# Optimization experiments

Measured on AMD Instinct MI355X. Metric: run time of the kernel, lower is better.

## Reference

```python
import jax, jax.numpy as jnp
import numpy as np

B = 256
MAXN = 1000
EPG = 7813
K, K1, K2 = 30, 3, 27


def setup_inputs():
    counts = np.where(np.arange(B) % 2 == 0, MAXN, 800).astype(np.int64)
    NT = int(counts.sum())  # 230400 nodes
    offsets = np.concatenate([[0], np.cumsum(counts)[:-1]]).astype(np.int64)
    batch = np.repeat(np.arange(B, dtype=np.int64), counts)
    rng = np.random.RandomState(0)
    E = B * EPG
    gid = np.repeat(np.arange(B), EPG)
    n = counts[gid]
    src = (rng.rand(E) * n).astype(np.int64)
    dst = (src + 1 + (rng.rand(E) * (n - 1)).astype(np.int64)) % n  # no self loops
    edge_index = np.stack([offsets[gid] + src, offsets[gid] + dst])
    key = jax.random.key(0)
    ks = jax.random.split(key, 8)
    def lin(k, fi, fo):
        return jax.random.normal(k, (fi, fo), jnp.float32) / np.sqrt(float(fi))
    return {
        'x': jax.random.normal(ks[0], (NT, 128), jnp.float32),
        'edge_index': jnp.asarray(edge_index),
        'batch': jnp.asarray(batch),
        'W1': lin(ks[1], 128, 64), 'b1': jnp.zeros(64, jnp.float32),
        'W2': lin(ks[2], 64, 64), 'b2': jnp.zeros(64, jnp.float32),
        'W3': lin(ks[3], 64, 64), 'b3': jnp.zeros(64, jnp.float32),
        'W4': lin(ks[4], 64, 1), 'b4': jnp.zeros(1, jnp.float32),
        'conv5_w': jax.random.normal(ks[5], (64, 1, 193), jnp.float32) / np.sqrt(193.0),
        'conv5_b': jnp.zeros(64, jnp.float32),
        'conv6_w': jax.random.normal(ks[6], (64, 64, 5), jnp.float32) / np.sqrt(320.0),
        'conv6_b': jnp.zeros(64, jnp.float32),
        'fc_w': lin(ks[7], 704, 1600), 'fc_b': jnp.zeros(1600, jnp.float32),
        'num_graphs': B,
        'max_num_nodes': MAXN,
    }


def _gcn(h_in, W, b, row, col, w_edge, self_w, N):
    h = h_in @ W
    agg = jax.ops.segment_sum(h[row] * w_edge[:, None], col, num_segments=N)
    return agg + self_w[:, None] * h + b


def _forward(x, edge_index, batch, W1, b1, W2, b2, W3, b3, W4, b4, conv5_w, conv5_b, conv6_w, conv6_b, fc_w, fc_b, num_graphs, max_num_nodes):
    N = x.shape[0]
    row, col = edge_index[0], edge_index[1]
    # GCN symmetric normalization with implicit self loops: deg = in-degree + 1
    deg = jax.ops.segment_sum(jnp.ones(row.shape[0], x.dtype), col, num_segments=N) + 1.0
    dis = jax.lax.rsqrt(deg)
    w_edge = dis[row] * dis[col]
    self_w = dis * dis
    x1 = jnp.tanh(_gcn(x, W1, b1, row, col, w_edge, self_w, N))
    x2 = jnp.tanh(_gcn(x1, W2, b2, row, col, w_edge, self_w, N))
    x3 = jnp.tanh(_gcn(x2, W3, b3, row, col, w_edge, self_w, N))
    x4 = jnp.tanh(_gcn(x3, W4, b4, row, col, w_edge, self_w, N))
    xc = jnp.concatenate([x1, x2, x3, x4], axis=-1)  # [N, 193]
    D = xc.shape[1]
    Bn, maxN = num_graphs, max_num_nodes
    # to_dense_batch with fill_value = min - 1
    num_nodes = jax.ops.segment_sum(jnp.ones(N, jnp.int32), batch, num_segments=Bn)
    cum = jnp.concatenate([jnp.zeros(1, jnp.int32), jnp.cumsum(num_nodes)])
    fill = xc.min() - 1.0
    idx = jnp.arange(N) - cum[batch] + batch.astype(jnp.int32) * maxN
    dense = jnp.full((Bn * maxN, D), fill, xc.dtype).at[idx].set(xc).reshape(Bn, maxN, D)
    # SortPooling: sort nodes per graph by last channel, descending
    order = jnp.argsort(-dense[:, :, -1], axis=-1)
    dense = jnp.take_along_axis(dense, order[:, :, None], axis=1)
    x_sort = dense[:, :K2]
    x_sort = jnp.where(x_sort == fill, 0.0, x_sort).reshape(Bn, K2 * D)
    # SimilarityPooling on residual nodes: sim[i] = sum_j ||x_i - x_j||^2 over first min(num_nodes, Nr) rows
    res = dense[:, K2:]  # [B, Nr, D]
    Nr = maxN - K2
    nv = jnp.minimum(num_nodes, Nr)
    mask = jnp.arange(Nr)[None, :] < nv[:, None]
    sq = jnp.sum(res * res, axis=-1)  # [B, Nr]
    Srow = jnp.sum(jnp.where(mask[:, :, None], res, 0.0), axis=1)  # [B, D]
    Tsum = jnp.sum(jnp.where(mask, sq, 0.0), axis=1)  # [B]
    nf = nv.astype(xc.dtype)
    sim = nf[:, None] * sq + Tsum[:, None] - 2.0 * jnp.einsum('bnd,bd->bn', res, Srow)
    sim = jnp.where(mask, sim, -jnp.inf)
    _, top = jax.lax.top_k(sim, K1)  # first K1 rows of the descending sort
    x_simi = jnp.take_along_axis(res, top[:, :, None], axis=1).reshape(Bn, K1 * D)
    pooled = jnp.concatenate([x_sort, x_simi], axis=1)  # [B, K*D] = [B, 5790]
    # 1D conv head
    h = pooled[:, None, :]
    h = jax.nn.relu(jax.lax.conv_general_dilated(h, conv5_w, (D,), 'VALID', dimension_numbers=('NCH', 'OIH', 'NCH')) + conv5_b[None, :, None])  # [B,64,30]
    h = h.reshape(Bn, 64, K // 2, 2).max(axis=-1)  # MaxPool1d(2,2) -> [B,64,15]
    h = jax.nn.relu(jax.lax.conv_general_dilated(h, conv6_w, (1,), 'VALID', dimension_numbers=('NCH', 'OIH', 'NCH')) + conv6_b[None, :, None])  # [B,64,11]
    h = h.reshape(Bn, -1)  # [B, 704]
    return jax.nn.relu(h @ fc_w + fc_b)  # dropout is identity in eval mode


def reference(x, edge_index, batch, W1, b1, W2, b2, W3, b3, W4, b4, conv5_w, conv5_b, conv6_w, conv6_b, fc_w, fc_b, num_graphs, max_num_nodes):
    return _forward(x, edge_index, batch, W1, b1, W2, b2, W3, b3, W4, b4, conv5_w, conv5_b, conv6_w, conv6_b, fc_w, fc_b, num_graphs, max_num_nodes)
```

## Files before the change

kernel.cpp:

```cpp
#include <hip/hip_runtime.h>
#include <float.h>
#include <limits.h>

static const int BG    = 256;
static const int SORTN = 1024;
static const int DF    = 193;
static const int K2C   = 27;
static const int K1C   = 3;
static const int NRESC = 973;
static const int PLEN  = 5790;
static const int GPARTS= 8;
static const int MAXE  = 8192;

#define DEV static __device__ __forceinline__

DEV float warp_sum64(float v){
#pragma unroll
  for (int o = 1; o < 64; o <<= 1) v += __shfl_xor(v, o);
  return v;
}
DEV float warp_min64(float v){
#pragma unroll
  for (int o = 1; o < 64; o <<= 1) v = fminf(v, __shfl_xor(v, o));
  return v;
}
DEV float feat_at(const float* __restrict__ x1, const float* __restrict__ x2,
                  const float* __restrict__ x3, const float* __restrict__ x4,
                  int node, int d){
  if (d < 64)  return x1[node*64 + d];
  if (d < 128) return x2[node*64 + (d-64)];
  if (d < 192) return x3[node*64 + (d-128)];
  return x4[node];
}
DEV int xcd_swizzle(int bid, int nwg){
  int q = nwg >> 3, r = nwg & 7;
  int x = bid & 7, i = bid >> 3;
  return ((x < r) ? x*(q+1) : r*(q+1) + (x-r)*q) + i;
}

__global__ __launch_bounds__(256) void k_bounds(const int* __restrict__ batch, int* __restrict__ goff, int NT){
  int i = blockIdx.x*256 + threadIdx.x;
  if (i < NT){
    if (i == 0 || batch[i] != batch[i-1]) goff[batch[i]] = i;
    if (i == NT-1) goff[BG] = NT;
  }
}
__global__ void k_gcount(const int* __restrict__ goff, int* __restrict__ gcount){
  int g = blockIdx.x*256 + threadIdx.x;
  if (g < BG) gcount[g] = goff[g+1] - goff[g];
}

__global__ __launch_bounds__(1024) void k_build(const int* __restrict__ rows, const int* __restrict__ cols,
                                                const int* __restrict__ gcount, const int* __restrict__ goff,
                                                float* __restrict__ dis, int* __restrict__ csr_off,
                                                int* __restrict__ csr_src, float* __restrict__ csr_w,
                                                int NT, int E, int epg){
  __shared__ int   lsrc[MAXE];
  __shared__ float lw[MAXE];
  __shared__ int   cnt[1024];
  __shared__ int   offl[1024];
  __shared__ int   cur[1024];
  __shared__ float disl[1024];
  __shared__ int   sm[1024];
  int g = blockIdx.x, tid = threadIdx.x;
  int n = gcount[g], base = goff[g];
  int ebase = g*epg;
  cnt[tid] = 0;
  __syncthreads();
  for (int i = tid; i < epg; i += 1024)
    atomicAdd(&cnt[cols[ebase+i] - base], 1);
  __syncthreads();
  if (tid < n){
    float d = 1.0f / sqrtf((float)cnt[tid] + 1.0f);
    disl[tid] = d;
    dis[base + tid] = d;
  }
  sm[tid] = cnt[tid]; __syncthreads();
  for (int o = 1; o < 1024; o <<= 1){
    int add = (tid >= o) ? sm[tid - o] : 0;
    __syncthreads(); sm[tid] += add; __syncthreads();
  }
  int excl = (tid > 0) ? sm[tid - 1] : 0;
  offl[tid] = excl; cur[tid] = excl;
  __syncthreads();
  if (tid < n) csr_off[base + tid] = ebase + offl[tid];
  if (g == BG - 1 && tid == 0) csr_off[NT] = E;
  for (int i = tid; i < epg; i += 1024){
    int r = rows[ebase + i], c = cols[ebase + i];
    float w = disl[r - base] * disl[c - base];
    int pos = atomicAdd(&cur[c - base], 1);
    lsrc[pos] = r;
    lw[pos]   = w;
  }
  __syncthreads();
  if (tid < n){
    int s0 = offl[tid];
    int s1 = (tid + 1 < n) ? offl[tid + 1] : epg;
    for (int i = s0 + 1; i < s1; i++){
      int ks = lsrc[i]; float kw = lw[i];
      int j = i - 1;
      while (j >= s0 && lsrc[j] > ks){ lsrc[j+1] = lsrc[j]; lw[j+1] = lw[j]; j--; }
      lsrc[j+1] = ks; lw[j+1] = kw;
    }
  }
  __syncthreads();
  for (int i = tid; i < epg; i += 1024){
    csr_src[ebase + i] = lsrc[i];
    csr_w[ebase + i]   = lw[i];
  }
}

template<int K>
__global__ __launch_bounds__(256) void k_gemm(const float* __restrict__ X, const float* __restrict__ W,
                                              float* __restrict__ H, int NT){
  const int BK = 32, KP = 36, NC = K/BK, TR = 128;
  __shared__ __align__(16) float xL[TR*KP];
  __shared__ __align__(16) float wL[BK*64];
  int tid = threadIdx.x;
  int rbase = blockIdx.x * TR;
  float4 px[4], pw[2];
  auto pre = [&](int c){
    int k0 = c*BK;
#pragma unroll
    for (int q = 0; q < 4; q++){
      int p = q*256 + tid;
      int row = p >> 3, c4 = p & 7;
      int gr = rbase + row;
      float4 v = make_float4(0.f,0.f,0.f,0.f);
      if (gr < NT) v = *((const float4*)&X[(size_t)gr*K + k0 + c4*4]);
      px[q] = v;
    }
#pragma unroll
    for (int j = 0; j < 2; j++){
      int i = tid*2 + j;
      int kr = i >> 4, cc = (i & 15)*4;
      pw[j] = *((const float4*)&W[(size_t)(k0 + kr)*64 + cc]);
    }
  };
  pre(0);
  int r0 = tid >> 3;
  int cg = (tid & 7) * 8;
  float acc[4][8];
#pragma unroll
  for (int i = 0; i < 4; i++)
#pragma unroll
    for (int j = 0; j < 8; j++) acc[i][j] = 0.f;
  for (int c = 0; c < NC; c++){
    if (c > 0) __syncthreads();
#pragma unroll
    for (int q = 0; q < 4; q++){
      int p = q*256 + tid;
      int row = p >> 3, c4 = p & 7;
      *((float4*)&xL[row*KP + c4*4]) = px[q];
    }
#pragma unroll
    for (int j = 0; j < 2; j++){
      int i = tid*2 + j;
      int kr = i >> 4, cc = (i & 15)*4;
      *((float4*)&wL[kr*64 + cc]) = pw[j];
    }
    if (c + 1 < NC) pre(c + 1);
    __syncthreads();
    for (int kq = 0; kq < BK; kq += 4){
      float4 xr[4];
#pragma unroll
      for (int i = 0; i < 4; i++) xr[i] = *((const float4*)&xL[(r0 + 32*i)*KP + kq]);
#pragma unroll
      for (int kk = 0; kk < 4; kk++){
        float4 wa = *((const float4*)&wL[(kq+kk)*64 + cg]);
        float4 wb = *((const float4*)&wL[(kq+kk)*64 + cg + 4]);
#pragma unroll
        for (int i = 0; i < 4; i++){
          float xv = (kk==0)?xr[i].x:(kk==1)?xr[i].y:(kk==2)?xr[i].z:xr[i].w;
          acc[i][0] = fmaf(xv, wa.x, acc[i][0]);
          acc[i][1] = fmaf(xv, wa.y, acc[i][1]);
          acc[i][2] = fmaf(xv, wa.z, acc[i][2]);
          acc[i][3] = fmaf(xv, wa.w, acc[i][3]);
          acc[i][4] = fmaf(xv, wb.x, acc[i][4]);
          acc[i][5] = fmaf(xv, wb.y, acc[i][5]);
          acc[i][6] = fmaf(xv, wb.z, acc[i][6]);
          acc[i][7] = fmaf(xv, wb.w, acc[i][7]);
        }
      }
    }
  }
#pragma unroll
  for (int i = 0; i < 4; i++){
    int gr = rbase + r0 + 32*i;
    if (gr < NT){
      float4 oa = make_float4(acc[i][0], acc[i][1], acc[i][2], acc[i][3]);
      float4 ob = make_float4(acc[i][4], acc[i][5], acc[i][6], acc[i][7]);
      *((float4*)&H[(size_t)gr*64 + cg])     = oa;
      *((float4*)&H[(size_t)gr*64 + cg + 4]) = ob;
    }
  }
}

template<bool FUSE_DOT>
__global__ __launch_bounds__(256) void k_agg(const float* __restrict__ H, const int* __restrict__ off,
                                             const int* __restrict__ srcs, const float* __restrict__ ws,
                                             const float* __restrict__ dis, const float* __restrict__ bias,
                                             const float* __restrict__ W4, float* __restrict__ Xout,
                                             float* __restrict__ H4, int NT, int nwg){
  int sbid = xcd_swizzle(blockIdx.x, nwg);
  int wv   = threadIdx.x >> 6;
  int lane = threadIdx.x & 63;
  int sub  = lane >> 4;
  int ql   = lane & 15;
  int node = sbid*16 + wv*4 + sub;
  if (node >= NT) return;
  int s0 = off[node], s1 = off[node+1];
  float4 a0=make_float4(0,0,0,0),a1=a0,a2=a0,a3=a0,a4=a0,a5=a0,a6=a0,a7=a0;
  int cb = ql*4;
  int e = s0;
  for (; e + 8 <= s1; e += 8){
    int   i0=srcs[e],  i1=srcs[e+1], i2=srcs[e+2], i3=srcs[e+3];
    int   i4=srcs[e+4],i5=srcs[e+5], i6=srcs[e+6], i7=srcs[e+7];
    float w0=ws[e],  w1=ws[e+1], w2=ws[e+2], w3=ws[e+3];
    float w4=ws[e+4],w5=ws[e+5], w6=ws[e+6], w7=ws[e+7];
    float4 h0=*((const float4*)&H[(size_t)i0*64+cb]);
    float4 h1=*((const float4*)&H[(size_t)i1*64+cb]);
    float4 h2=*((const float4*)&H[(size_t)i2*64+cb]);
    float4 h3=*((const float4*)&H[(size_t)i3*64+cb]);
    float4 h4=*((const float4*)&H[(size_t)i4*64+cb]);
    float4 h5=*((const float4*)&H[(size_t)i5*64+cb]);
    float4 h6=*((const float4*)&H[(size_t)i6*64+cb]);
    float4 h7=*((const float4*)&H[(size_t)i7*64+cb]);
    a0.x=fmaf(w0,h0.x,a0.x); a0.y=fmaf(w0,h0.y,a0.y); a0.z=fmaf(w0,h0.z,a0.z); a0.w=fmaf(w0,h0.w,a0.w);
    a1.x=fmaf(w1,h1.x,a1.x); a1.y=fmaf(w1,h1.y,a1.y); a1.z=fmaf(w1,h1.z,a1.z); a1.w=fmaf(w1,h1.w,a1.w);
    a2.x=fmaf(w2,h2.x,a2.x); a2.y=fmaf(w2,h2.y,a2.y); a2.z=fmaf(w2,h2.z,a2.z); a2.w=fmaf(w2,h2.w,a2.w);
    a3.x=fmaf(w3,h3.x,a3.x); a3.y=fmaf(w3,h3.y,a3.y); a3.z=fmaf(w3,h3.z,a3.z); a3.w=fmaf(w3,h3.w,a3.w);
    a4.x=fmaf(w4,h4.x,a4.x); a4.y=fmaf(w4,h4.y,a4.y); a4.z=fmaf(w4,h4.z,a4.z); a4.w=fmaf(w4,h4.w,a4.w);
    a5.x=fmaf(w5,h5.x,a5.x); a5.y=fmaf(w5,h5.y,a5.y); a5.z=fmaf(w5,h5.z,a5.z); a5.w=fmaf(w5,h5.w,a5.w);
    a6.x=fmaf(w6,h6.x,a6.x); a6.y=fmaf(w6,h6.y,a6.y); a6.z=fmaf(w6,h6.z,a6.z); a6.w=fmaf(w6,h6.w,a6.w);
    a7.x=fmaf(w7,h7.x,a7.x); a7.y=fmaf(w7,h7.y,a7.y); a7.z=fmaf(w7,h7.z,a7.z); a7.w=fmaf(w7,h7.w,a7.w);
  }
  if (e + 4 <= s1){
    int   i0=srcs[e],  i1=srcs[e+1], i2=srcs[e+2], i3=srcs[e+3];
    float w0=ws[e],  w1=ws[e+1], w2=ws[e+2], w3=ws[e+3];
    float4 h0=*((const float4*)&H[(size_t)i0*64+cb]);
    float4 h1=*((const float4*)&H[(size_t)i1*64+cb]);
    float4 h2=*((const float4*)&H[(size_t)i2*64+cb]);
    float4 h3=*((const float4*)&H[(size_t)i3*64+cb]);
    a0.x=fmaf(w0,h0.x,a0.x); a0.y=fmaf(w0,h0.y,a0.y); a0.z=fmaf(w0,h0.z,a0.z); a0.w=fmaf(w0,h0.w,a0.w);
    a1.x=fmaf(w1,h1.x,a1.x); a1.y=fmaf(w1,h1.y,a1.y); a1.z=fmaf(w1,h1.z,a1.z); a1.w=fmaf(w1,h1.w,a1.w);
    a2.x=fmaf(w2,h2.x,a2.x); a2.y=fmaf(w2,h2.y,a2.y); a2.z=fmaf(w2,h2.z,a2.z); a2.w=fmaf(w2,h2.w,a2.w);
    a3.x=fmaf(w3,h3.x,a3.x); a3.y=fmaf(w3,h3.y,a3.y); a3.z=fmaf(w3,h3.z,a3.z); a3.w=fmaf(w3,h3.w,a3.w);
    e += 4;
  }
  if (e < s1){
    float w = ws[e]; float4 h=*((const float4*)&H[(size_t)srcs[e]*64+cb]);
    a4.x=fmaf(w,h.x,a4.x); a4.y=fmaf(w,h.y,a4.y); a4.z=fmaf(w,h.z,a4.z); a4.w=fmaf(w,h.w,a4.w);
  }
  if (e + 1 < s1){
    float w = ws[e+1]; float4 h=*((const float4*)&H[(size_t)srcs[e+1]*64+cb]);
    a5.x=fmaf(w,h.x,a5.x); a5.y=fmaf(w,h.y,a5.y); a5.z=fmaf(w,h.z,a5.z); a5.w=fmaf(w,h.w,a5.w);
  }
  if (e + 2 < s1){
    float w = ws[e+2]; float4 h=*((const float4*)&H[(size_t)srcs[e+2]*64+cb]);
    a6.x=fmaf(w,h.x,a6.x); a6.y=fmaf(w,h.y,a6.y); a6.z=fmaf(w,h.z,a6.z); a6.w=fmaf(w,h.w,a6.w);
  }
  float4 acc;
  acc.x = ((a0.x+a1.x)+(a2.x+a3.x)) + ((a4.x+a5.x)+(a6.x+a7.x));
  acc.y = ((a0.y+a1.y)+(a2.y+a3.y)) + ((a4.y+a5.y)+(a6.y+a7.y));
  acc.z = ((a0.z+a1.z)+(a2.z+a3.z)) + ((a4.z+a5.z)+(a6.z+a7.z));
  acc.w = ((a0.w+a1.w)+(a2.w+a3.w)) + ((a4.w+a5.w)+(a6.w+a7.w));
  float dv = dis[node];
  float dv2 = dv*dv;
  float4 hs = *((const float4*)&H[(size_t)node*64 + cb]);
  float4 bb = *((const float4*)&bias[cb]);
  float4 t;
  t.x = tanhf(acc.x + dv2*hs.x + bb.x);
  t.y = tanhf(acc.y + dv2*hs.y + bb.y);
  t.z = tanhf(acc.z + dv2*hs.z + bb.z);
  t.w = tanhf(acc.w + dv2*hs.w + bb.w);
  *((float4*)&Xout[(size_t)node*64 + cb]) = t;
  if (FUSE_DOT){
    float4 w4v = *((const float4*)&W4[cb]);
    float p = t.x*w4v.x + t.y*w4v.y + t.z*w4v.z + t.w*w4v.w;
#pragma unroll
    for (int o = 1; o < 16; o <<= 1) p += __shfl_xor(p, o);
    if (ql == 0) H4[node] = p;
  }
}

__global__ __launch_bounds__(256) void k_agg1(const float* __restrict__ H4, const int* __restrict__ off,
                                              const int* __restrict__ srcs, const float* __restrict__ ws,
                                              const float* __restrict__ dis, const float* __restrict__ b4,
                                              float* __restrict__ x4, int NT){
  int v = blockIdx.x*256 + threadIdx.x;
  if (v >= NT) return;
  int s0 = off[v], s1 = off[v+1];
  float acc = 0.f;
  for (int e = s0; e < s1; e++) acc = fmaf(ws[e], H4[srcs[e]], acc);
  float dv = dis[v];
  x4[v] = tanhf(acc + dv*dv*H4[v] + b4[0]);
}

__global__ __launch_bounds__(256) void k_stats(const float* __restrict__ x1, const float* __restrict__ x2,
                                               const float* __restrict__ x3, const float* __restrict__ x4,
                                               const int* __restrict__ gcount, const int* __restrict__ goff,
                                               float* __restrict__ sqv, float* __restrict__ gpart,
                                               float* __restrict__ bmin){
  __shared__ float sm[256];
  __shared__ float wm[4];
  int g = blockIdx.x, p = blockIdx.y, tid = threadIdx.x;
  int wv = tid >> 6, lane = tid & 63;
  int n = gcount[g], base = goff[g];
  int n0 = (int)(((long long)n * p) / GPARTS);
  int n1 = (int)(((long long)n * (p+1)) / GPARTS);
  float a1 = 0.f, a2 = 0.f, a3 = 0.f;
  float a4 = 0.f, asq = 0.f;
  float mn = FLT_MAX;
  for (int i = n0 + wv; i < n1; i += 4){
    size_t node = (size_t)(base + i);
    float v1 = x1[node*64 + lane];
    float v2 = x2[node*64 + lane];
    float v3 = x3[node*64 + lane];
    a1 += v1; a2 += v2; a3 += v3;
    mn = fminf(mn, fminf(fminf(v1, v2), v3));
    float s = warp_sum64(v1*v1 + v2*v2 + v3*v3);
    if (lane == 0){
      float d = x4[node];
      float sq = s + d*d;
      sqv[node] = sq;
      a4 += d; asq += sq;
      mn = fminf(mn, d);
    }
  }
  float* out = &gpart[(size_t)(g*GPARTS + p) * 194];
  sm[tid] = a1; __syncthreads();
  if (tid < 64) out[tid] = sm[tid] + sm[tid+64] + sm[tid+128] + sm[tid+192];
  __syncthreads();
  sm[tid] = a2; __syncthreads();
  if (tid < 64) out[64 + tid] = sm[tid] + sm[tid+64] + sm[tid+128] + sm[tid+192];
  __syncthreads();
  sm[tid] = a3; __syncthreads();
  if (tid < 64) out[128 + tid] = sm[tid] + sm[tid+64] + sm[tid+128] + sm[tid+192];
  __syncthreads();
  sm[tid] = (lane == 0) ? a4 : 0.f; __syncthreads();
  for (int o = 128; o > 0; o >>= 1){
    if (tid < o) sm[tid] += sm[tid + o];
    __syncthreads();
  }
  if (tid == 0) out[192] = sm[0];
  __syncthreads();
  sm[tid] = (lane == 0) ? asq : 0.f; __syncthreads();
  for (int o = 128; o > 0; o >>= 1){
    if (tid < o) sm[tid] += sm[tid + o];
    __syncthreads();
  }
  if (tid == 0) out[193] = sm[0];
  mn = warp_min64(mn);
  if (lane == 0) wm[wv] = mn;
  __syncthreads();
  if (tid == 0)
    bmin[g*GPARTS + p] = fminf(fminf(wm[0], wm[1]), fminf(wm[2], wm[3]));
}
__global__ __launch_bounds__(256) void k_min2(const float* __restrict__ bmin, int nb, float* __restrict__ minv){
  __shared__ float sm[256];
  float m = FLT_MAX;
  for (int i = threadIdx.x; i < nb; i += 256) m = fminf(m, bmin[i]);
  sm[threadIdx.x] = m; __syncthreads();
  for (int o = 128; o > 0; o >>= 1){
    if (threadIdx.x < o) sm[threadIdx.x] = fminf(sm[threadIdx.x], sm[threadIdx.x + o]);
    __syncthreads();
  }
  if (threadIdx.x == 0) minv[0] = sm[0];
}
__global__ __launch_bounds__(256) void k_gcomb(const float* __restrict__ gpart, float* __restrict__ gstats){
  int g = blockIdx.x, c = threadIdx.x;
  if (c < 194){
    float s = 0.f;
    for (int p = 0; p < GPARTS; p++) s += gpart[(size_t)(g*GPARTS + p)*194 + c];
    gstats[g*194 + c] = s;
  }
}

__global__ __launch_bounds__(256) void k_sort(const float* __restrict__ x4, const int* __restrict__ gcount,
                                              const int* __restrict__ goff, int* __restrict__ sidxg,
                                              int* __restrict__ rank){
  __shared__ float sval[SORTN];
  __shared__ int   sidx[SORTN];
  int g = blockIdx.x, tid = threadIdx.x;
  int n = gcount[g], base = goff[g];
  for (int i = tid; i < SORTN; i += 256){
    sval[i] = (i < n) ? x4[base + i] : -FLT_MAX;
    sidx[i] = i;
  }
  __syncthreads();
  for (int k = 2; k <= SORTN; k <<= 1){
    for (int j = k >> 1; j > 0; j >>= 1){
      for (int t = tid; t < SORTN/2; t += 256){
        int i   = 2*t - (t & (j - 1));
        int ixj = i | j;
        bool up = ((i & k) == 0);
        float va = sval[i], vb = sval[ixj];
        int   ia = sidx[i], ib = sidx[ixj];
        bool aBeforeB = (va > vb) || (va == vb && ia < ib);
        bool bBeforeA = (vb > va) || (vb == va && ib < ia);
        bool doswap = up ? bBeforeA : aBeforeB;
        if (doswap){ sval[i] = vb; sval[ixj] = va; sidx[i] = ib; sidx[ixj] = ia; }
      }
      __syncthreads();
    }
  }
  for (int i = tid; i < SORTN; i += 256) sidxg[g*SORTN + i] = sidx[i];
  for (int i = tid; i < n; i += 256) rank[base + sidx[i]] = i;
}

__global__ __launch_bounds__(256) void k_top27(const float* __restrict__ x1, const float* __restrict__ x2,
                                               const float* __restrict__ x3, const float* __restrict__ x4,
                                               const float* __restrict__ sqv, const int* __restrict__ gcount,
                                               const int* __restrict__ goff, const int* __restrict__ sidxg,
                                               const float* __restrict__ gstats, const float* __restrict__ minv,
                                               float* __restrict__ Srow, float* __restrict__ TS,
                                               float* __restrict__ pooled){
  __shared__ int   t27n[K2C];
  __shared__ float srow_s[DF];
  int g = blockIdx.x, tid = threadIdx.x;
  int n = gcount[g], base = goff[g];
  float fill = minv[0] - 1.0f;
  int nv = (n < NRESC) ? n : NRESC;
  int nreal = n - K2C;
  int nfill = nv - nreal;
  if (tid < K2C) t27n[tid] = base + sidxg[g*SORTN + tid];
  __syncthreads();
  if (tid < DF){
    float s = 0.f;
    for (int r = 0; r < K2C; r++) s += feat_at(x1, x2, x3, x4, t27n[r], tid);
    float v = gstats[g*194 + tid] - s + (float)nfill * fill;
    srow_s[tid] = v;
    Srow[g*DF + tid] = v;
  }
  for (int i = tid; i < K2C*DF; i += 256){
    int r = i / DF, d = i - r*DF;
    pooled[(size_t)g*PLEN + i] = feat_at(x1, x2, x3, x4, t27n[r], d);
  }
  __syncthreads();
  if (tid == 0){
    float t27sq = 0.f;
    for (int r = 0; r < K2C; r++) t27sq += sqv[t27n[r]];
    float sqfill = (float)DF * fill * fill;
    float Tsum = gstats[g*194 + 193] - t27sq + (float)nfill * sqfill;
    float ssum = 0.f;
    for (int d = 0; d < DF; d++) ssum += srow_s[d];
    float nf = (float)nv;
    float simfill = nf * sqfill + Tsum - 2.0f * fill * ssum;
    TS[g*2 + 0] = Tsum;
    TS[g*2 + 1] = simfill;
  }
}

__global__ __launch_bounds__(256) void k_sim(const float* __restrict__ x1, const float* __restrict__ x2,
                                             const float* __restrict__ x3, const float* __restrict__ x4,
                                             const float* __restrict__ sqv, const int* __restrict__ batch,
                                             const int* __restrict__ gcount, const int* __restrict__ rank,
                                             const float* __restrict__ Srow, const float* __restrict__ TS,
                                             float* __restrict__ sim, int NT){
  int wid  = blockIdx.x*4 + (threadIdx.x >> 6);
  int lane = threadIdx.x & 63;
  if (wid >= NT) return;
  if (rank[wid] < K2C) return;
  int g = batch[wid];
  float a = x1[(size_t)wid*64 + lane];
  float b = x2[(size_t)wid*64 + lane];
  float c = x3[(size_t)wid*64 + lane];
  float s1 = Srow[g*DF + lane];
  float s2 = Srow[g*DF + 64 + lane];
  float s3 = Srow[g*DF + 128 + lane];
  float dot = warp_sum64(a*s1 + b*s2 + c*s3);
  if (lane == 0){
    float d = x4[wid];
    dot += d * Srow[g*DF + 192];
    int n = gcount[g];
    float nf = (float)((n < NRESC) ? n : NRESC);
    sim[wid] = nf * sqv[wid] + TS[g*2] - 2.0f * dot;
  }
}

DEV void top3_insert(float v, int j, float* tv, int* tj){
  if (v > tv[0] || (v == tv[0] && j < tj[0])){
    tv[2]=tv[1]; tj[2]=tj[1]; tv[1]=tv[0]; tj[1]=tj[0]; tv[0]=v; tj[0]=j;
  } else if (v > tv[1] || (v == tv[1] && j < tj[1])){
    tv[2]=tv[1]; tj[2]=tj[1]; tv[1]=v; tj[1]=j;
  } else if (v > tv[2] || (v == tv[2] && j < tj[2])){
    tv[2]=v; tj[2]=j;
  }
}
__global__ __launch_bounds__(256) void k_top3(const float* __restrict__ x1, const float* __restrict__ x2,
                                              const float* __restrict__ x3, const float* __restrict__ x4,
                                              const float* __restrict__ sim, const int* __restrict__ rank,
                                              const int* __restrict__ gcount, const int* __restrict__ goff,
                                              const int* __restrict__ sidxg, const float* __restrict__ TS,
                                              const float* __restrict__ minv, float* __restrict__ pooled){
  __shared__ float lv[256*3];
  __shared__ int   lj[256*3];
  __shared__ int   fsel[3];
  int g = blockIdx.x, tid = threadIdx.x;
  int n = gcount[g], base = goff[g];
  float fill = minv[0] - 1.0f;
  int nv = (n < NRESC) ? n : NRESC;
  int nreal = n - K2C;
  int nfill = nv - nreal;
  float tv[3] = {-FLT_MAX, -FLT_MAX, -FLT_MAX};
  int   tj[3] = {INT_MAX, INT_MAX, INT_MAX};
  for (int i = tid; i < n; i += 256){
    int node = base + i;
    int r = rank[node];
    if (r >= K2C) top3_insert(sim[node], r - K2C, tv, tj);
  }
#pragma unroll
  for (int q = 0; q < 3; q++){ lv[tid*3 + q] = tv[q]; lj[tid*3 + q] = tj[q]; }
  __syncthreads();
  for (int o = 128; o >= 1; o >>= 1){
    if (tid < o){
#pragma unroll
      for (int q = 0; q < 3; q++)
        top3_insert(lv[(tid + o)*3 + q], lj[(tid + o)*3 + q], tv, tj);
#pragma unroll
      for (int q = 0; q < 3; q++){ lv[tid*3 + q] = tv[q]; lj[tid*3 + q] = tj[q]; }
    }
    __syncthreads();
  }
  if (tid == 0){
    float simfill = TS[g*2 + 1];
    int ninj = (nfill < 3) ? nfill : 3;
    for (int q = 0; q < ninj; q++) top3_insert(simfill, nreal + q, tv, tj);
    fsel[0] = tj[0]; fsel[1] = tj[1]; fsel[2] = tj[2];
  }
  __syncthreads();
  for (int i = tid; i < K1C*DF; i += 256){
    int m = i / DF, d = i - m*DF;
    int j = fsel[m];
    float v;
    if (j < nreal){
      int node = base + sidxg[g*SORTN + K2C + j];
      v = feat_at(x1, x2, x3, x4, node, d);
    } else {
      v = fill;
    }
    pooled[(size_t)g*PLEN + K2C*DF + i] = v;
  }
}

__global__ __launch_bounds__(256) void k_head(const float* __restrict__ pooled, const float* __restrict__ w5,
                                              const float* __restrict__ b5, const float* __restrict__ w6,
                                              const float* __restrict__ b6, float* __restrict__ h6){
  __shared__ float smem[21760];
  float* pl  = smem;
  float* w5T = smem + 5790;
  float* h5  = smem + 18528;
  float* mx  = smem;
  float* w6T = smem + 960;
  int g = blockIdx.x, tid = threadIdx.x;
  for (int i = tid; i < PLEN; i += 256) pl[i] = pooled[(size_t)g*PLEN + i];
  for (int i = tid; i < 64*DF; i += 256){
    int o = i / DF, d = i - o*DF;
    w5T[d*66 + o] = w5[i];
  }
  __syncthreads();
  int o = tid & 63, tg = tid >> 6;
  for (int t = tg; t < 30; t += 4){
    const float* pr = &pl[t*DF];
    float a0=0.f, a1=0.f, a2=0.f, a3=0.f;
    for (int d = 0; d < 192; d += 4){
      a0 = fmaf(pr[d],   w5T[(d)*66 + o],   a0);
      a1 = fmaf(pr[d+1], w5T[(d+1)*66 + o], a1);
      a2 = fmaf(pr[d+2], w5T[(d+2)*66 + o], a2);
      a3 = fmaf(pr[d+3], w5T[(d+3)*66 + o], a3);
    }
    a0 = fmaf(pr[192], w5T[192*66 + o], a0);
    float acc = b5[o] + ((a0 + a1) + (a2 + a3));
    h5[t*64 + o] = fmaxf(acc, 0.f);
  }
  __syncthreads();
  for (int i = tid; i < 15*64; i += 256){
    int p = i >> 6, oo = i & 63;
    mx[i] = fmaxf(h5[(2*p)*64 + oo], h5[(2*p + 1)*64 + oo]);
  }
  __syncthreads();
  for (int i = tid; i < 64*64*5; i += 256){
    int oo = i / 320, rem = i - oo*320;
    w6T[rem*65 + oo] = w6[i];
  }
  __syncthreads();
  for (int t = tg; t < 11; t += 4){
    float a0=0.f, a1=0.f, a2=0.f, a3=0.f;
    for (int ii = 0; ii < 64; ii += 4){
#pragma unroll
      for (int k = 0; k < 5; k++){
        a0 = fmaf(mx[(t+k)*64 + ii],   w6T[((ii)*5   + k)*65 + o], a0);
        a1 = fmaf(mx[(t+k)*64 + ii+1], w6T[((ii+1)*5 + k)*65 + o], a1);
        a2 = fmaf(mx[(t+k)*64 + ii+2], w6T[((ii+2)*5 + k)*65 + o], a2);
        a3 = fmaf(mx[(t+k)*64 + ii+3], w6T[((ii+3)*5 + k)*65 + o], a3);
      }
    }
    float acc = b6[o] + ((a0 + a1) + (a2 + a3));
    h6[(size_t)g*704 + o*11 + t] = fmaxf(acc, 0.f);
  }
}

__global__ __launch_bounds__(256) void k_fc(const float* __restrict__ h6, const float* __restrict__ fw,
                                            const float* __restrict__ fb, float* __restrict__ out){
  int j  = blockIdx.x*64 + (threadIdx.x & 63);
  int b0 = __builtin_amdgcn_readfirstlane(blockIdx.y*16 + (threadIdx.x >> 6)*4);
  const float* h0p = h6 + (size_t)b0*704;
  const float* h1p = h0p + 704;
  const float* h2p = h0p + 1408;
  const float* h3p = h0p + 2112;
  float a0e=0.f,a0o=0.f,a1e=0.f,a1o=0.f,a2e=0.f,a2o=0.f,a3e=0.f,a3o=0.f;
#pragma unroll 4
  for (int k = 0; k < 704; k += 2){
    float w0 = fw[(size_t)k*1600 + j];
    float w1 = fw[(size_t)k*1600 + 1600 + j];
    a0e = fmaf(h0p[k], w0, a0e); a0o = fmaf(h0p[k+1], w1, a0o);
    a1e = fmaf(h1p[k], w0, a1e); a1o = fmaf(h1p[k+1], w1, a1o);
    a2e = fmaf(h2p[k], w0, a2e); a2o = fmaf(h2p[k+1], w1, a2o);
    a3e = fmaf(h3p[k], w0, a3e); a3o = fmaf(h3p[k+1], w1, a3o);
  }
  float fbj = fb[j];
  out[(size_t)b0*1600 + j]       = fmaxf(a0e + a0o + fbj, 0.f);
  out[(size_t)(b0+1)*1600 + j]   = fmaxf(a1e + a1o + fbj, 0.f);
  out[(size_t)(b0+2)*1600 + j]   = fmaxf(a2e + a2o + fbj, 0.f);
  out[(size_t)(b0+3)*1600 + j]   = fmaxf(a3e + a3o + fbj, 0.f);
}

extern "C" void kernel_launch(void* const* d_in, const int* in_sizes, int n_in,
                              void* d_out, int out_size, void* d_ws, size_t ws_size,
                              hipStream_t stream){
  const float* x    = (const float*)d_in[0];
  const int*   ei   = (const int*)d_in[1];
  const int*   batch= (const int*)d_in[2];
  const float* W1 = (const float*)d_in[3];  const float* b1 = (const float*)d_in[4];
  const float* W2 = (const float*)d_in[5];  const float* b2 = (const float*)d_in[6];
  const float* W3 = (const float*)d_in[7];  const float* b3 = (const float*)d_in[8];
  const float* W4 = (const float*)d_in[9];  const float* b4 = (const float*)d_in[10];
  const float* w5 = (const float*)d_in[11]; const float* b5 = (const float*)d_in[12];
  const float* w6 = (const float*)d_in[13]; const float* b6 = (const float*)d_in[14];
  const float* fw = (const float*)d_in[15]; const float* fb = (const float*)d_in[16];
  float* out = (float*)d_out;

  const int NT = in_sizes[2];
  const int E  = in_sizes[1] / 2;
  const int epg = E / BG;
  const int* rows = ei;
  const int* cols = ei + E;

  char* ws = (char*)d_ws;
  size_t off = 0;
  auto alloc = [&](size_t bytes) -> char* {
    off = (off + 255) & ~(size_t)255;
    char* p = ws + off;
    off += bytes;
    return p;
  };

  int*      gcount  = (int*)     alloc(BG * 4);
  int*      goff    = (int*)     alloc((BG + 1) * 4);
  float*    minv    = (float*)   alloc(4);
  float*    bmin    = (float*)   alloc((size_t)BG * GPARTS * 4);
  float*    dis     = (float*)   alloc((size_t)NT * 4);
  int*      csr_off = (int*)     alloc((size_t)(NT + 1) * 4);
  int*      csr_src = (int*)     alloc((size_t)E * 4);
  float*    csr_w   = (float*)   alloc((size_t)E * 4);
  float*    Hbuf    = (float*)   alloc((size_t)NT * 64 * 4);
  float*    x1      = (float*)   alloc((size_t)NT * 64 * 4);
  float*    x2      = (float*)   alloc((size_t)NT * 64 * 4);
  float*    x3      = (float*)   alloc((size_t)NT * 64 * 4);
  float*    x4      = (float*)   alloc((size_t)NT * 4);
  float*    H4      = (float*)   alloc((size_t)NT * 4);
  float*    sqv     = (float*)   alloc((size_t)NT * 4);
  float*    simv    = (float*)   alloc((size_t)NT * 4);
  int*      rank    = (int*)     alloc((size_t)NT * 4);
  int*      sidxg   = (int*)     alloc((size_t)BG * SORTN * 4);
  float*    gpart   = (float*)   alloc((size_t)BG * GPARTS * 194 * 4);
  float*    gstats  = (float*)   alloc((size_t)BG * 194 * 4);
  float*    Srow    = (float*)   alloc((size_t)BG * DF * 4);
  float*    TS      = (float*)   alloc((size_t)BG * 2 * 4);
  float*    pooled  = (float*)   alloc((size_t)BG * PLEN * 4);
  float*    h6      = (float*)   alloc((size_t)BG * 704 * 4);

  const int gridNT = (NT + 255) / 256;
  const int gridA  = (NT + 15) / 16;
  const int gridS  = (NT + 3) / 4;

  k_bounds<<<gridNT, 256, 0, stream>>>(batch, goff, NT);
  k_gcount<<<1, 256, 0, stream>>>(goff, gcount);
  k_build<<<BG, 1024, 0, stream>>>(rows, cols, gcount, goff, dis, csr_off, csr_src, csr_w, NT, E, epg);

  const int gridG = (NT + 127) / 128;

  k_gemm<128><<<gridG, 256, 0, stream>>>(x, W1, Hbuf, NT);
  k_agg<false><<<gridA, 256, 0, stream>>>(Hbuf, csr_off, csr_src, csr_w, dis, b1, W4, x1, H4, NT, gridA);
  k_gemm<64><<<gridG, 256, 0, stream>>>(x1, W2, Hbuf, NT);
  k_agg<false><<<gridA, 256, 0, stream>>>(Hbuf, csr_off, csr_src, csr_w, dis, b2, W4, x2, H4, NT, gridA);
  k_gemm<64><<<gridG, 256, 0, stream>>>(x2, W3, Hbuf, NT);
  k_agg<true><<<gridA, 256, 0, stream>>>(Hbuf, csr_off, csr_src, csr_w, dis, b3, W4, x3, H4, NT, gridA);
  k_agg1<<<gridNT, 256, 0, stream>>>(H4, csr_off, csr_src, csr_w, dis, b4, x4, NT);

  k_stats<<<dim3(BG, GPARTS), 256, 0, stream>>>(x1, x2, x3, x4, gcount, goff, sqv, gpart, bmin);
  k_min2<<<1, 256, 0, stream>>>(bmin, BG*GPARTS, minv);
  k_gcomb<<<BG, 256, 0, stream>>>(gpart, gstats);
  k_sort<<<BG, 256, 0, stream>>>(x4, gcount, goff, sidxg, rank);
  k_top27<<<BG, 256, 0, stream>>>(x1, x2, x3, x4, sqv, gcount, goff, sidxg, gstats, minv, Srow, TS, pooled);
  k_sim<<<gridS, 256, 0, stream>>>(x1, x2, x3, x4, sqv, batch, gcount, rank, Srow, TS, simv, NT);
  k_top3<<<BG, 256, 0, stream>>>(x1, x2, x3, x4, simv, rank, gcount, goff, sidxg, TS, minv, pooled);

  k_head<<<BG, 256, 0, stream>>>(pooled, w5, b5, w6, b6, h6);
  k_fc<<<dim3(25, 16), 256, 0, stream>>>(h6, fw, fb, out);
}
```

Measured before the change: 637.4 us.

## Fuse next-layer 64x64 GEMM into GCN aggregation kernels

```diff
diff --git a/kernel.cpp b/kernel.cpp
--- a/kernel.cpp
+++ b/kernel.cpp
@@ -196,22 +196,12 @@
   }
 }
 
-template<bool FUSE_DOT>
-__global__ __launch_bounds__(256) void k_agg(const float* __restrict__ H, const int* __restrict__ off,
-                                             const int* __restrict__ srcs, const float* __restrict__ ws,
-                                             const float* __restrict__ dis, const float* __restrict__ bias,
-                                             const float* __restrict__ W4, float* __restrict__ Xout,
-                                             float* __restrict__ H4, int NT, int nwg){
-  int sbid = xcd_swizzle(blockIdx.x, nwg);
-  int wv   = threadIdx.x >> 6;
-  int lane = threadIdx.x & 63;
-  int sub  = lane >> 4;
-  int ql   = lane & 15;
-  int node = sbid*16 + wv*4 + sub;
-  if (node >= NT) return;
+DEV float4 agg_node(const float* __restrict__ H, const int* __restrict__ off,
+                    const int* __restrict__ srcs, const float* __restrict__ ws,
+                    const float* __restrict__ dis, const float* __restrict__ bias,
+                    int node, int cb){
   int s0 = off[node], s1 = off[node+1];
   float4 a0=make_float4(0,0,0,0),a1=a0,a2=a0,a3=a0,a4=a0,a5=a0,a6=a0,a7=a0;
-  int cb = ql*4;
   int e = s0;
   for (; e + 8 <= s1; e += 8){
     int   i0=srcs[e],  i1=srcs[e+1], i2=srcs[e+2], i3=srcs[e+3];
@@ -274,14 +264,92 @@
   t.y = tanhf(acc.y + dv2*hs.y + bb.y);
   t.z = tanhf(acc.z + dv2*hs.z + bb.z);
   t.w = tanhf(acc.w + dv2*hs.w + bb.w);
+  return t;
+}
+
+__global__ __launch_bounds__(256) void k_aggf(const float* __restrict__ H, const int* __restrict__ off,
+                                              const int* __restrict__ srcs, const float* __restrict__ ws,
+                                              const float* __restrict__ dis, const float* __restrict__ bias,
+                                              const float* __restrict__ Wn, float* __restrict__ Xout,
+                                              float* __restrict__ Hnext, int NT, int nwg){
+  __shared__ __align__(16) float zL[64*68];
+  __shared__ __align__(16) float wL[64*64];
+  int sbid = xcd_swizzle(blockIdx.x, nwg);
+  int tid = threadIdx.x;
+  int wv = tid >> 6, lane = tid & 63, sub = lane >> 4, ql = lane & 15;
+  int cb = ql*4;
+  int nbase = sbid*64;
+#pragma unroll
+  for (int q = 0; q < 4; q++)
+    *((float4*)&wL[(q*256+tid)*4]) = ((const float4*)Wn)[q*256+tid];
+  for (int it = 0; it < 4; it++){
+    int ln = it*16 + wv*4 + sub;
+    int node = nbase + ln;
+    if (node < NT){
+      float4 t = agg_node(H, off, srcs, ws, dis, bias, node, cb);
+      *((float4*)&Xout[(size_t)node*64 + cb]) = t;
+      *((float4*)&zL[ln*68 + cb]) = t;
+    }
+  }
+  __syncthreads();
+  int rr = tid >> 3;
+  int cg = (tid & 7) * 8;
+  float acc[2][8];
+#pragma unroll
+  for (int i = 0; i < 2; i++)
+#pragma unroll
+    for (int j = 0; j < 8; j++) acc[i][j] = 0.f;
+  for (int k0 = 0; k0 < 64; k0 += 4){
+    float4 xr0 = *((const float4*)&zL[rr*68 + k0]);
+    float4 xr1 = *((const float4*)&zL[(rr+32)*68 + k0]);
+#pragma unroll
+    for (int kk = 0; kk < 4; kk++){
+      float4 wa = *((const float4*)&wL[(k0+kk)*64 + cg]);
+      float4 wb = *((const float4*)&wL[(k0+kk)*64 + cg + 4]);
+      float x0 = (kk==0)?xr0.x:(kk==1)?xr0.y:(kk==2)?xr0.z:xr0.w;
+      float x1v= (kk==0)?xr1.x:(kk==1)?xr1.y:(kk==2)?xr1.z:xr1.w;
+      acc[0][0]=fmaf(x0,wa.x,acc[0][0]); acc[0][1]=fmaf(x0,wa.y,acc[0][1]);
+      acc[0][2]=fmaf(x0,wa.z,acc[0][2]); acc[0][3]=fmaf(x0,wa.w,acc[0][3]);
+      acc[0][4]=fmaf(x0,wb.x,acc[0][4]); acc[0][5]=fmaf(x0,wb.y,acc[0][5]);
+      acc[0][6]=fmaf(x0,wb.z,acc[0][6]); acc[0][7]=fmaf(x0,wb.w,acc[0][7]);
+      acc[1][0]=fmaf(x1v,wa.x,acc[1][0]); acc[1][1]=fmaf(x1v,wa.y,acc[1][1]);
+      acc[1][2]=fmaf(x1v,wa.z,acc[1][2]); acc[1][3]=fmaf(x1v,wa.w,acc[1][3]);
+      acc[1][4]=fmaf(x1v,wb.x,acc[1][4]); acc[1][5]=fmaf(x1v,wb.y,acc[1][5]);
+      acc[1][6]=fmaf(x1v,wb.z,acc[1][6]); acc[1][7]=fmaf(x1v,wb.w,acc[1][7]);
+    }
+  }
+#pragma unroll
+  for (int i = 0; i < 2; i++){
+    int gr = nbase + rr + 32*i;
+    if (gr < NT){
+      float4 oa = make_float4(acc[i][0], acc[i][1], acc[i][2], acc[i][3]);
+      float4 ob = make_float4(acc[i][4], acc[i][5], acc[i][6], acc[i][7]);
+      *((float4*)&Hnext[(size_t)gr*64 + cg])     = oa;
+      *((float4*)&Hnext[(size_t)gr*64 + cg + 4]) = ob;
+    }
+  }
+}
+
+__global__ __launch_bounds__(256) void k_agg3(const float* __restrict__ H, const int* __restrict__ off,
+                                              const int* __restrict__ srcs, const float* __restrict__ ws,
+                                              const float* __restrict__ dis, const float* __restrict__ bias,
+                                              const float* __restrict__ W4, float* __restrict__ Xout,
+                                              float* __restrict__ H4, int NT, int nwg){
+  int sbid = xcd_swizzle(blockIdx.x, nwg);
+  int wv   = threadIdx.x >> 6;
+  int lane = threadIdx.x & 63;
+  int sub  = lane >> 4;
+  int ql   = lane & 15;
+  int node = sbid*16 + wv*4 + sub;
+  if (node >= NT) return;
+  int cb = ql*4;
+  float4 t = agg_node(H, off, srcs, ws, dis, bias, node, cb);
   *((float4*)&Xout[(size_t)node*64 + cb]) = t;
-  if (FUSE_DOT){
-    float4 w4v = *((const float4*)&W4[cb]);
-    float p = t.x*w4v.x + t.y*w4v.y + t.z*w4v.z + t.w*w4v.w;
-#pragma unroll
-    for (int o = 1; o < 16; o <<= 1) p += __shfl_xor(p, o);
-    if (ql == 0) H4[node] = p;
-  }
+  float4 w4v = *((const float4*)&W4[cb]);
+  float p = t.x*w4v.x + t.y*w4v.y + t.z*w4v.z + t.w*w4v.w;
+#pragma unroll
+  for (int o = 1; o < 16; o <<= 1) p += __shfl_xor(p, o);
+  if (ql == 0) H4[node] = p;
 }
 
 __global__ __launch_bounds__(256) void k_agg1(const float* __restrict__ H4, const int* __restrict__ off,
@@ -664,7 +732,8 @@
   int*      csr_off = (int*)     alloc((size_t)(NT + 1) * 4);
   int*      csr_src = (int*)     alloc((size_t)E * 4);
   float*    csr_w   = (float*)   alloc((size_t)E * 4);
-  float*    Hbuf    = (float*)   alloc((size_t)NT * 64 * 4);
+  float*    HbufA   = (float*)   alloc((size_t)NT * 64 * 4);
+  float*    HbufB   = (float*)   alloc((size_t)NT * 64 * 4);
   float*    x1      = (float*)   alloc((size_t)NT * 64 * 4);
   float*    x2      = (float*)   alloc((size_t)NT * 64 * 4);
   float*    x3      = (float*)   alloc((size_t)NT * 64 * 4);
@@ -682,21 +751,19 @@
   float*    h6      = (float*)   alloc((size_t)BG * 704 * 4);
 
   const int gridNT = (NT + 255) / 256;
+  const int gridF  = (NT + 63) / 64;
   const int gridA  = (NT + 15) / 16;
   const int gridS  = (NT + 3) / 4;
+  const int gridG  = (NT + 127) / 128;
 
   k_bounds<<<gridNT, 256, 0, stream>>>(batch, goff, NT);
   k_gcount<<<1, 256, 0, stream>>>(goff, gcount);
   k_build<<<BG, 1024, 0, stream>>>(rows, cols, gcount, goff, dis, csr_off, csr_src, csr_w, NT, E, epg);
 
-  const int gridG = (NT + 127) / 128;
-
-  k_gemm<128><<<gridG, 256, 0, stream>>>(x, W1, Hbuf, NT);
-  k_agg<false><<<gridA, 256, 0, stream>>>(Hbuf, csr_off, csr_src, csr_w, dis, b1, W4, x1, H4, NT, gridA);
-  k_gemm<64><<<gridG, 256, 0, stream>>>(x1, W2, Hbuf, NT);
-  k_agg<false><<<gridA, 256, 0, stream>>>(Hbuf, csr_off, csr_src, csr_w, dis, b2, W4, x2, H4, NT, gridA);
-  k_gemm<64><<<gridG, 256, 0, stream>>>(x2, W3, Hbuf, NT);
-  k_agg<true><<<gridA, 256, 0, stream>>>(Hbuf, csr_off, csr_src, csr_w, dis, b3, W4, x3, H4, NT, gridA);
+  k_gemm<128><<<gridG, 256, 0, stream>>>(x, W1, HbufA, NT);
+  k_aggf<<<gridF, 256, 0, stream>>>(HbufA, csr_off, csr_src, csr_w, dis, b1, W2, x1, HbufB, NT, gridF);
+  k_aggf<<<gridF, 256, 0, stream>>>(HbufB, csr_off, csr_src, csr_w, dis, b2, W3, x2, HbufA, NT, gridF);
+  k_agg3<<<gridA, 256, 0, stream>>>(HbufA, csr_off, csr_src, csr_w, dis, b3, W4, x3, H4, NT, gridA);
   k_agg1<<<gridNT, 256, 0, stream>>>(H4, csr_off, csr_src, csr_w, dis, b4, x4, NT);
 
   k_stats<<<dim3(BG, GPARTS), 256, 0, stream>>>(x1, x2, x3, x4, gcount, goff, sqv, gpart, bmin);
```

Result: no change. 635.7 us (-0.3%).

## Aggregate GCN layers per graph from LDS-staged feature halves

Applied to the files above, without the earlier changes.

```diff
diff --git a/kernel.cpp b/kernel.cpp
--- a/kernel.cpp
+++ b/kernel.cpp
@@ -11,6 +11,8 @@
 static const int PLEN  = 5790;
 static const int GPARTS= 8;
 static const int MAXE  = 8192;
+static const int MAXN  = 1000;
+static const int HLP   = 36;
 
 #define DEV static __device__ __forceinline__
 
@@ -31,11 +33,6 @@
   if (d < 128) return x2[node*64 + (d-64)];
   if (d < 192) return x3[node*64 + (d-128)];
   return x4[node];
-}
-DEV int xcd_swizzle(int bid, int nwg){
-  int q = nwg >> 3, r = nwg & 7;
-  int x = bid & 7, i = bid >> 3;
-  return ((x < r) ? x*(q+1) : r*(q+1) + (x-r)*q) + i;
 }
 
 __global__ __launch_bounds__(256) void k_bounds(const int* __restrict__ batch, int* __restrict__ goff, int NT){
@@ -196,91 +193,80 @@
   }
 }
 
-template<bool FUSE_DOT>
-__global__ __launch_bounds__(256) void k_agg(const float* __restrict__ H, const int* __restrict__ off,
-                                             const int* __restrict__ srcs, const float* __restrict__ ws,
-                                             const float* __restrict__ dis, const float* __restrict__ bias,
-                                             const float* __restrict__ W4, float* __restrict__ Xout,
-                                             float* __restrict__ H4, int NT, int nwg){
-  int sbid = xcd_swizzle(blockIdx.x, nwg);
-  int wv   = threadIdx.x >> 6;
-  int lane = threadIdx.x & 63;
-  int sub  = lane >> 4;
-  int ql   = lane & 15;
-  int node = sbid*16 + wv*4 + sub;
-  if (node >= NT) return;
-  int s0 = off[node], s1 = off[node+1];
-  float4 a0=make_float4(0,0,0,0),a1=a0,a2=a0,a3=a0,a4=a0,a5=a0,a6=a0,a7=a0;
-  int cb = ql*4;
-  int e = s0;
-  for (; e + 8 <= s1; e += 8){
-    int   i0=srcs[e],  i1=srcs[e+1], i2=srcs[e+2], i3=srcs[e+3];
-    int   i4=srcs[e+4],i5=srcs[e+5], i6=srcs[e+6], i7=srcs[e+7];
-    float w0=ws[e],  w1=ws[e+1], w2=ws[e+2], w3=ws[e+3];
-    float w4=ws[e+4],w5=ws[e+5], w6=ws[e+6], w7=ws[e+7];
-    float4 h0=*((const float4*)&H[(size_t)i0*64+cb]);
-    float4 h1=*((const float4*)&H[(size_t)i1*64+cb]);
-    float4 h2=*((const float4*)&H[(size_t)i2*64+cb]);
-    float4 h3=*((const float4*)&H[(size_t)i3*64+cb]);
-    float4 h4=*((const float4*)&H[(size_t)i4*64+cb]);
-    float4 h5=*((const float4*)&H[(size_t)i5*64+cb]);
-    float4 h6=*((const float4*)&H[(size_t)i6*64+cb]);
-    float4 h7=*((const float4*)&H[(size_t)i7*64+cb]);
-    a0.x=fmaf(w0,h0.x,a0.x); a0.y=fmaf(w0,h0.y,a0.y); a0.z=fmaf(w0,h0.z,a0.z); a0.w=fmaf(w0,h0.w,a0.w);
-    a1.x=fmaf(w1,h1.x,a1.x); a1.y=fmaf(w1,h1.y,a1.y); a1.z=fmaf(w1,h1.z,a1.z); a1.w=fmaf(w1,h1.w,a1.w);
-    a2.x=fmaf(w2,h2.x,a2.x); a2.y=fmaf(w2,h2.y,a2.y); a2.z=fmaf(w2,h2.z,a2.z); a2.w=fmaf(w2,h2.w,a2.w);
-    a3.x=fmaf(w3,h3.x,a3.x); a3.y=fmaf(w3,h3.y,a3.y); a3.z=fmaf(w3,h3.z,a3.z); a3.w=fmaf(w3,h3.w,a3.w);
-    a4.x=fmaf(w4,h4.x,a4.x); a4.y=fmaf(w4,h4.y,a4.y); a4.z=fmaf(w4,h4.z,a4.z); a4.w=fmaf(w4,h4.w,a4.w);
-    a5.x=fmaf(w5,h5.x,a5.x); a5.y=fmaf(w5,h5.y,a5.y); a5.z=fmaf(w5,h5.z,a5.z); a5.w=fmaf(w5,h5.w,a5.w);
-    a6.x=fmaf(w6,h6.x,a6.x); a6.y=fmaf(w6,h6.y,a6.y); a6.z=fmaf(w6,h6.z,a6.z); a6.w=fmaf(w6,h6.w,a6.w);
-    a7.x=fmaf(w7,h7.x,a7.x); a7.y=fmaf(w7,h7.y,a7.y); a7.z=fmaf(w7,h7.z,a7.z); a7.w=fmaf(w7,h7.w,a7.w);
-  }
-  if (e + 4 <= s1){
-    int   i0=srcs[e],  i1=srcs[e+1], i2=srcs[e+2], i3=srcs[e+3];
-    float w0=ws[e],  w1=ws[e+1], w2=ws[e+2], w3=ws[e+3];
-    float4 h0=*((const float4*)&H[(size_t)i0*64+cb]);
-    float4 h1=*((const float4*)&H[(size_t)i1*64+cb]);
-    float4 h2=*((const float4*)&H[(size_t)i2*64+cb]);
-    float4 h3=*((const float4*)&H[(size_t)i3*64+cb]);
-    a0.x=fmaf(w0,h0.x,a0.x); a0.y=fmaf(w0,h0.y,a0.y); a0.z=fmaf(w0,h0.z,a0.z); a0.w=fmaf(w0,h0.w,a0.w);
-    a1.x=fmaf(w1,h1.x,a1.x); a1.y=fmaf(w1,h1.y,a1.y); a1.z=fmaf(w1,h1.z,a1.z); a1.w=fmaf(w1,h1.w,a1.w);
-    a2.x=fmaf(w2,h2.x,a2.x); a2.y=fmaf(w2,h2.y,a2.y); a2.z=fmaf(w2,h2.z,a2.z); a2.w=fmaf(w2,h2.w,a2.w);
-    a3.x=fmaf(w3,h3.x,a3.x); a3.y=fmaf(w3,h3.y,a3.y); a3.z=fmaf(w3,h3.z,a3.z); a3.w=fmaf(w3,h3.w,a3.w);
-    e += 4;
-  }
-  if (e < s1){
-    float w = ws[e]; float4 h=*((const float4*)&H[(size_t)srcs[e]*64+cb]);
-    a4.x=fmaf(w,h.x,a4.x); a4.y=fmaf(w,h.y,a4.y); a4.z=fmaf(w,h.z,a4.z); a4.w=fmaf(w,h.w,a4.w);
-  }
-  if (e + 1 < s1){
-    float w = ws[e+1]; float4 h=*((const float4*)&H[(size_t)srcs[e+1]*64+cb]);
-    a5.x=fmaf(w,h.x,a5.x); a5.y=fmaf(w,h.y,a5.y); a5.z=fmaf(w,h.z,a5.z); a5.w=fmaf(w,h.w,a5.w);
-  }
-  if (e + 2 < s1){
-    float w = ws[e+2]; float4 h=*((const float4*)&H[(size_t)srcs[e+2]*64+cb]);
-    a6.x=fmaf(w,h.x,a6.x); a6.y=fmaf(w,h.y,a6.y); a6.z=fmaf(w,h.z,a6.z); a6.w=fmaf(w,h.w,a6.w);
-  }
-  float4 acc;
-  acc.x = ((a0.x+a1.x)+(a2.x+a3.x)) + ((a4.x+a5.x)+(a6.x+a7.x));
-  acc.y = ((a0.y+a1.y)+(a2.y+a3.y)) + ((a4.y+a5.y)+(a6.y+a7.y));
-  acc.z = ((a0.z+a1.z)+(a2.z+a3.z)) + ((a4.z+a5.z)+(a6.z+a7.z));
-  acc.w = ((a0.w+a1.w)+(a2.w+a3.w)) + ((a4.w+a5.w)+(a6.w+a7.w));
-  float dv = dis[node];
-  float dv2 = dv*dv;
-  float4 hs = *((const float4*)&H[(size_t)node*64 + cb]);
-  float4 bb = *((const float4*)&bias[cb]);
-  float4 t;
-  t.x = tanhf(acc.x + dv2*hs.x + bb.x);
-  t.y = tanhf(acc.y + dv2*hs.y + bb.y);
-  t.z = tanhf(acc.z + dv2*hs.z + bb.z);
-  t.w = tanhf(acc.w + dv2*hs.w + bb.w);
-  *((float4*)&Xout[(size_t)node*64 + cb]) = t;
-  if (FUSE_DOT){
-    float4 w4v = *((const float4*)&W4[cb]);
-    float p = t.x*w4v.x + t.y*w4v.y + t.z*w4v.z + t.w*w4v.w;
-#pragma unroll
-    for (int o = 1; o < 16; o <<= 1) p += __shfl_xor(p, o);
-    if (ql == 0) H4[node] = p;
+template<bool DO_H4>
+__global__ __launch_bounds__(1024) void k_aggL(const float* __restrict__ H, const int* __restrict__ off,
+                                               const int* __restrict__ srcs, const float* __restrict__ ws,
+                                               const float* __restrict__ dis, const float* __restrict__ bias,
+                                               const float* __restrict__ W4,
+                                               float* __restrict__ Xout, float* __restrict__ H4,
+                                               const int* __restrict__ gcount, const int* __restrict__ goff){
+  __shared__ __align__(16) float hl[MAXN*HLP];
+  __shared__ float pdot[1024];
+  int g = blockIdx.x, tid = threadIdx.x;
+  int n = gcount[g], base = goff[g];
+  int l = tid & 7, gid = tid >> 3;
+  int co = l*4;
+#pragma unroll
+  for (int pass = 0; pass < 2; pass++){
+    int cbase = pass*32;
+    if (pass == 1) __syncthreads();
+    for (int i = tid; i < n*8; i += 1024){
+      int r = i >> 3, q = i & 7;
+      *((float4*)&hl[r*HLP + q*4]) =
+        *((const float4*)&H[(size_t)(base + r)*64 + cbase + q*4]);
+    }
+    __syncthreads();
+    for (int v = gid; v < n; v += 128){
+      int node = base + v;
+      int s0 = off[node], s1 = off[node+1];
+      float4 a0 = make_float4(0.f,0.f,0.f,0.f), a1 = a0, a2 = a0, a3 = a0;
+      int e = s0;
+      for (; e + 4 <= s1; e += 4){
+        int   r0 = srcs[e]   - base, r1 = srcs[e+1] - base;
+        int   r2 = srcs[e+2] - base, r3 = srcs[e+3] - base;
+        float w0 = ws[e], w1 = ws[e+1], w2 = ws[e+2], w3 = ws[e+3];
+        float4 h0 = *((const float4*)&hl[r0*HLP + co]);
+        float4 h1 = *((const float4*)&hl[r1*HLP + co]);
+        float4 h2 = *((const float4*)&hl[r2*HLP + co]);
+        float4 h3 = *((const float4*)&hl[r3*HLP + co]);
+        a0.x=fmaf(w0,h0.x,a0.x); a0.y=fmaf(w0,h0.y,a0.y); a0.z=fmaf(w0,h0.z,a0.z); a0.w=fmaf(w0,h0.w,a0.w);
+        a1.x=fmaf(w1,h1.x,a1.x); a1.y=fmaf(w1,h1.y,a1.y); a1.z=fmaf(w1,h1.z,a1.z); a1.w=fmaf(w1,h1.w,a1.w);
+        a2.x=fmaf(w2,h2.x,a2.x); a2.y=fmaf(w2,h2.y,a2.y); a2.z=fmaf(w2,h2.z,a2.z); a2.w=fmaf(w2,h2.w,a2.w);
+        a3.x=fmaf(w3,h3.x,a3.x); a3.y=fmaf(w3,h3.y,a3.y); a3.z=fmaf(w3,h3.z,a3.z); a3.w=fmaf(w3,h3.w,a3.w);
+      }
+      for (; e < s1; e++){
+        int r = srcs[e] - base; float w = ws[e];
+        float4 h = *((const float4*)&hl[r*HLP + co]);
+        a0.x=fmaf(w,h.x,a0.x); a0.y=fmaf(w,h.y,a0.y); a0.z=fmaf(w,h.z,a0.z); a0.w=fmaf(w,h.w,a0.w);
+      }
+      float4 acc;
+      acc.x = (a0.x+a1.x)+(a2.x+a3.x);
+      acc.y = (a0.y+a1.y)+(a2.y+a3.y);
+      acc.z = (a0.z+a1.z)+(a2.z+a3.z);
+      acc.w = (a0.w+a1.w)+(a2.w+a3.w);
+      float dv = dis[node];
+      float dv2 = dv*dv;
+      float4 hs = *((const float4*)&hl[v*HLP + co]);
+      float4 bb = *((const float4*)&bias[cbase + co]);
+      float4 t;
+      t.x = tanhf(acc.x + dv2*hs.x + bb.x);
+      t.y = tanhf(acc.y + dv2*hs.y + bb.y);
+      t.z = tanhf(acc.z + dv2*hs.z + bb.z);
+      t.w = tanhf(acc.w + dv2*hs.w + bb.w);
+      *((float4*)&Xout[(size_t)node*64 + cbase + co]) = t;
+      if (DO_H4){
+        float4 w4v = *((const float4*)&W4[cbase + co]);
+        float p = t.x*w4v.x + t.y*w4v.y + t.z*w4v.z + t.w*w4v.w;
+        p += __shfl_xor(p, 1);
+        p += __shfl_xor(p, 2);
+        p += __shfl_xor(p, 4);
+        if (pass == 0){
+          if (l == 0) pdot[v] = p;
+        } else {
+          if (l == 0) H4[node] = pdot[v] + p;
+        }
+      }
+    }
   }
 }
 
@@ -664,7 +650,8 @@
   int*      csr_off = (int*)     alloc((size_t)(NT + 1) * 4);
   int*      csr_src = (int*)     alloc((size_t)E * 4);
   float*    csr_w   = (float*)   alloc((size_t)E * 4);
-  float*    Hbuf    = (float*)   alloc((size_t)NT * 64 * 4);
+  float*    HbufA   = (float*)   alloc((size_t)NT * 64 * 4);
+  float*    HbufB   = (float*)   alloc((size_t)NT * 64 * 4);
   float*    x1      = (float*)   alloc((size_t)NT * 64 * 4);
   float*    x2      = (float*)   alloc((size_t)NT * 64 * 4);
   float*    x3      = (float*)   alloc((size_t)NT * 64 * 4);
@@ -682,21 +669,19 @@
   float*    h6      = (float*)   alloc((size_t)BG * 704 * 4);
 
   const int gridNT = (NT + 255) / 256;
-  const int gridA  = (NT + 15) / 16;
   const int gridS  = (NT + 3) / 4;
+  const int gridG  = (NT + 127) / 128;
 
   k_bounds<<<gridNT, 256, 0, stream>>>(batch, goff, NT);
   k_gcount<<<1, 256, 0, stream>>>(goff, gcount);
   k_build<<<BG, 1024, 0, stream>>>(rows, cols, gcount, goff, dis, csr_off, csr_src, csr_w, NT, E, epg);
 
-  const int gridG = (NT + 127) / 128;
-
-  k_gemm<128><<<gridG, 256, 0, stream>>>(x, W1, Hbuf, NT);
-  k_agg<false><<<gridA, 256, 0, stream>>>(Hbuf, csr_off, csr_src, csr_w, dis, b1, W4, x1, H4, NT, gridA);
-  k_gemm<64><<<gridG, 256, 0, stream>>>(x1, W2, Hbuf, NT);
-  k_agg<false><<<gridA, 256, 0, stream>>>(Hbuf, csr_off, csr_src, csr_w, dis, b2, W4, x2, H4, NT, gridA);
-  k_gemm<64><<<gridG, 256, 0, stream>>>(x2, W3, Hbuf, NT);
-  k_agg<true><<<gridA, 256, 0, stream>>>(Hbuf, csr_off, csr_src, csr_w, dis, b3, W4, x3, H4, NT, gridA);
+  k_gemm<128><<<gridG, 256, 0, stream>>>(x, W1, HbufA, NT);
+  k_aggL<false><<<BG, 1024, 0, stream>>>(HbufA, csr_off, csr_src, csr_w, dis, b1, W4, x1, H4, gcount, goff);
+  k_gemm<64><<<gridG, 256, 0, stream>>>(x1, W2, HbufB, NT);
+  k_aggL<false><<<BG, 1024, 0, stream>>>(HbufB, csr_off, csr_src, csr_w, dis, b2, W4, x2, H4, gcount, goff);
+  k_gemm<64><<<gridG, 256, 0, stream>>>(x2, W3, HbufA, NT);
+  k_aggL<true><<<BG, 1024, 0, stream>>>(HbufA, csr_off, csr_src, csr_w, dis, b3, W4, x3, H4, gcount, goff);
   k_agg1<<<gridNT, 256, 0, stream>>>(H4, csr_off, csr_src, csr_w, dis, b4, x4, NT);
 
   k_stats<<<dim3(BG, GPARTS), 256, 0, stream>>>(x1, x2, x3, x4, gcount, goff, sqv, gpart, bmin);
```

Measured after the change: 628.3 us. Within noise of the previous version (-1.4%).
